# Kernel tuning notes

Hardware: AMD Instinct MI355X
Metric: run time of the kernel (lower is better)

## Reference

```python
import jax, jax.numpy as jnp
import numpy as np

ALPHA = 0.2          # LeakyReLU negative slope
NEG_INF = -9e15      # mask fill value from the torch code


def _gat_layer(h, adj_mask, W, a):
    """Faithful GAT layer. The torch code builds an [m*m, 2F] tensor and
    multiplies by a [2F,1] vector; algebraically identical to splitting
    a into a_i (first F) and a_k (last F) and broadcasting:
    e[i,k] = leakyrelu(Wh[i] . a_i + Wh[k] . a_k).
    Dropout is identity in eval mode (training=False)."""
    Wh = h @ W                                   # [m, F]
    F_out = W.shape[1]
    s_i = Wh @ a[:F_out, 0]                      # [m]
    s_k = Wh @ a[F_out:, 0]                      # [m]
    e = jax.nn.leaky_relu(s_i[:, None] + s_k[None, :], negative_slope=ALPHA)  # [m, m]
    e = jnp.where(adj_mask > 0, e, NEG_INF)
    attention = jax.nn.softmax(e, axis=1)        # row-wise softmax
    return jax.nn.elu(attention @ Wh)            # [m, F]


def setup_inputs() -> dict:
    m, in_dim, hid, emb = 4096, 64, 64, 32
    key = jax.random.key(0)
    k = jax.random.split(key, 6)
    # xavier-uniform-like init, gain=1.414
    def xavier(kk, shape):
        fan_in, fan_out = shape[0], shape[1]
        bound = 1.414 * np.sqrt(6.0 / (fan_in + fan_out))
        return jax.random.uniform(kk, shape, jnp.float32, -bound, bound)
    return {
        "h0": jax.random.normal(k[0], (m, in_dim), jnp.float32),
        "adj_mask": jax.random.randint(k[1], (m, m), 0, 2, jnp.int32),
        "W1": xavier(k[2], (in_dim, hid)),
        "a1": xavier(k[3], (2 * hid, 1)),
        "W2": xavier(k[4], (hid, emb)),
        "a2": xavier(k[5], (2 * emb, 1)),
        "omega": xavier(jax.random.fold_in(key, 7), (2 * emb, 1)),
    }


def reference(h0, adj_mask, W1, a1, W2, a2, omega):
    h1 = _gat_layer(h0, adj_mask, W1, a1)        # [m, hid]
    hL = _gat_layer(h1, adj_mask, W2, a2)        # [m, emb]
    # pairwise link score: sigmoid(omega . [hL_i, hL_k]) -- same broadcast trick
    emb = hL.shape[1]
    p_i = hL @ omega[:emb, 0]                    # [m]
    p_k = hL @ omega[emb:, 0]                    # [m]
    pred_matrix = jax.nn.sigmoid(p_i[:, None] + p_k[None, :])  # [m, m]
    return pred_matrix, hL
```

## Files before the change

kernel.cpp:

```cpp
#include <hip/hip_runtime.h>
#include <hip/hip_bf16.h>
#include <math.h>

#define M 4096
#define ALPHA 0.2f
#define L2E 1.4426950408889634f
#define PACK_BLOCKS (M * M / 4 / 256)

typedef __attribute__((ext_vector_type(8))) short bf16x8_t;
typedef __attribute__((ext_vector_type(4))) float f32x4_t;

#define EXP2F(x) __builtin_amdgcn_exp2f(x)

__device__ inline unsigned short f2bf(float f) {
    unsigned int u = __float_as_uint(f);
    u = (u + 0x7fffu + ((u >> 16) & 1u)) >> 16;
    return (unsigned short)u;
}
__device__ inline unsigned short f2bf_fast(float f) {
    return (unsigned short)((__float_as_uint(f) + 0x8000u) >> 16);
}
__device__ inline size_t whb_idx(int i, int c, int NFB) {
    return (((size_t)(i >> 5) * NFB + (c >> 4)) * 64 +
            (((i & 31) >> 3) * 16 + (c & 15))) * 8 + (i & 7);
}

__global__ __launch_bounds__(256) void prep_fat_kernel(const int* __restrict__ adj,
                                                       unsigned int* __restrict__ packedT,
                                                       const float* __restrict__ h0,
                                                       const float* __restrict__ W1,
                                                       const float* __restrict__ a1,
                                                       unsigned short* __restrict__ WhB1,
                                                       float* __restrict__ si1,
                                                       float* __restrict__ sk1) {
    int lane = threadIdx.x & 63;
    if (blockIdx.x < PACK_BLOCKS) {
        int g = blockIdx.x * 256 + threadIdx.x;
        int4 av = ((const int4*)adj)[g];
        unsigned int nib = (av.x > 0 ? 1u : 0u) | (av.y > 0 ? 2u : 0u) |
                           (av.z > 0 ? 4u : 0u) | (av.w > 0 ? 8u : 0u);
        unsigned int sh = nib << ((lane & 7) * 4);
        sh |= __shfl_xor(sh, 1);
        sh |= __shfl_xor(sh, 2);
        sh |= __shfl_xor(sh, 4);
        if ((lane & 7) == 0) packedT[(size_t)((g >> 3) & 127) * M + (g >> 10)] = sh;
        return;
    }
    int wave = threadIdx.x >> 6;
    int i = (blockIdx.x - PACK_BLOCKS) * 4 + wave;
    float acc = 0.f;
#pragma unroll
    for (int j = 0; j < 64; j++)
        acc += h0[(size_t)i * 64 + j] * W1[j * 64 + lane];
    float vi = acc * a1[lane], vk = acc * a1[64 + lane];
#pragma unroll
    for (int off = 32; off; off >>= 1) { vi += __shfl_xor(vi, off); vk += __shfl_xor(vk, off); }
    if (lane == 0) { si1[i] = vi; sk1[i] = vk; }
    WhB1[whb_idx(i, lane, 4)] = f2bf(acc);
}

template <int F, bool FINAL>
__global__ __launch_bounds__(1024) void attn_fused_kernel(
    const unsigned short* __restrict__ WhB,
    const float* __restrict__ s_i, const float* __restrict__ s_k,
    const unsigned int* __restrict__ packedT,
    const float* __restrict__ W2, const float* __restrict__ a2,
    unsigned short* __restrict__ WhB2, float* __restrict__ si2, float* __restrict__ sk2,
    const float* __restrict__ omega, float* __restrict__ hL_out,
    float* __restrict__ p_i, float* __restrict__ p_k) {
    constexpr int NFB = F / 16;
    constexpr int NWAVE = 16;
    constexpr int WPW = (M / 32) / NWAVE;
    __shared__ unsigned int mask_lds[16][129];
    __shared__ float acc_lds[NWAVE][16][F + 1];
    __shared__ float sred[NWAVE][16];
    __shared__ float wred[NWAVE];
    __shared__ float h_lds[16][F + 1];

    int tid = threadIdx.x, wave = tid >> 6, lane = tid & 63;
    int R0 = blockIdx.x * 16;

    float m = -INFINITY;
#pragma unroll
    for (int t = 0; t < M / 1024; t++) m = fmaxf(m, s_k[tid + t * 1024]);
#pragma unroll
    for (int off = 32; off; off >>= 1) m = fmaxf(m, __shfl_xor(m, off));
    if (lane == 0) wred[wave] = m;
#pragma unroll
    for (int q = 0; q < 2; q++) {
        int lin = q * 1024 + tid;
        int st = lin >> 4, r = lin & 15;
        mask_lds[r][st] = packedT[(size_t)st * M + R0 + r];
    }
    __syncthreads();
    float skmax = wred[0];
#pragma unroll
    for (int w = 1; w < NWAVE; w++) skmax = fmaxf(skmax, wred[w]);

    int fl = lane & 15, kg = lane >> 4;
    int row = R0 + fl;
    float si = s_i[row];
    float xm = si + skmax;
    float rl2 = fmaxf(xm, ALPHA * xm) * L2E;
    f32x4_t acc[NFB];
#pragma unroll
    for (int fb = 0; fb < NFB; fb++) acc[fb] = (f32x4_t)0.f;
    float rsum = 0.f;
    const int kw0 = wave * WPW;
#pragma unroll
    for (int st = 0; st < WPW; st++) {
        int kb = (kw0 + st) * 32;
        float4 sa = *(const float4*)&s_k[kb + kg * 8];
        float4 sb = *(const float4*)&s_k[kb + kg * 8 + 4];
        unsigned int word = mask_lds[fl][kw0 + st];
        float sv[8] = { sa.x, sa.y, sa.z, sa.w, sb.x, sb.y, sb.z, sb.w };
        union { bf16x8_t v; unsigned short u[8]; } af;
#pragma unroll
        for (int j = 0; j < 8; j++) {
            float x = si + sv[j];
            float e = fmaxf(x, ALPHA * x);
            float p = EXP2F(fmaf(e, L2E, -rl2));
            p = ((word >> (kg * 8 + j)) & 1u) ? p : 0.f;
            rsum += p;
            af.u[j] = f2bf_fast(p);
        }
        const unsigned short* bp = WhB + (size_t)(kw0 + st) * (NFB * 512) + (size_t)lane * 8;
#pragma unroll
        for (int fb = 0; fb < NFB; fb++) {
            bf16x8_t bfrag = *(const bf16x8_t*)(bp + (size_t)fb * 512);
            acc[fb] = __builtin_amdgcn_mfma_f32_16x16x32_bf16(af.v, bfrag, acc[fb], 0, 0, 0);
        }
    }
    rsum += __shfl_xor(rsum, 16);
    rsum += __shfl_xor(rsum, 32);
    if (lane < 16) sred[wave][lane] = rsum;
#pragma unroll
    for (int fb = 0; fb < NFB; fb++)
#pragma unroll
        for (int r = 0; r < 4; r++)
            acc_lds[wave][kg * 4 + r][fb * 16 + fl] = acc[fb][r];
    __syncthreads();

    if (tid < 16 * F) {
        int r = tid / F, c = tid % F;
        float s = 0.f, S = 0.f;
#pragma unroll
        for (int w = 0; w < NWAVE; w++) { s += acc_lds[w][r][c]; S += sred[w][r]; }
        float h = S > 0.f ? s / S : 0.f;
        h = h > 0.f ? h : (__expf(h) - 1.f);
        h_lds[r][c] = h;
        if (FINAL) hL_out[(size_t)(R0 + r) * F + c] = h;
    }
    __syncthreads();

    if (tid < 512) {
        int r = tid >> 5, c = tid & 31;
        float vi, vk;
        if (!FINAL) {
            float w2 = 0.f;
#pragma unroll
            for (int f = 0; f < 64; f++) w2 += h_lds[r][f] * W2[f * 32 + c];
            WhB2[whb_idx(R0 + r, c, 2)] = f2bf(w2);
            vi = w2 * a2[c];
            vk = w2 * a2[32 + c];
        } else {
            float hv = h_lds[r][c];
            vi = hv * omega[c];
            vk = hv * omega[32 + c];
        }
#pragma unroll
        for (int off = 16; off; off >>= 1) { vi += __shfl_xor(vi, off); vk += __shfl_xor(vk, off); }
        if ((tid & 31) == 0) {
            if (!FINAL) { si2[R0 + r] = vi; sk2[R0 + r] = vk; }
            else        { p_i[R0 + r] = vi; p_k[R0 + r] = vk; }
        }
    }
}

__global__ __launch_bounds__(256) void pred_kernel(const float* __restrict__ p_i,
                                                   const float* __restrict__ p_k,
                                                   float* __restrict__ out) {
    int gid = blockIdx.x * 256 + threadIdx.x;
#pragma unroll
    for (int t = 0; t < 4; t++) {
        int idx4 = gid + t * (M * M / 16);
        int i = idx4 >> 10;
        int k4 = (idx4 & 1023) * 4;
        float pi = p_i[i];
        float4 pk = *(const float4*)&p_k[k4];
        float4 o;
        o.x = 1.f / (1.f + __expf(-(pi + pk.x)));
        o.y = 1.f / (1.f + __expf(-(pi + pk.y)));
        o.z = 1.f / (1.f + __expf(-(pi + pk.z)));
        o.w = 1.f / (1.f + __expf(-(pi + pk.w)));
        *(float4*)&out[(size_t)i * M + k4] = o;
    }
}

extern "C" void kernel_launch(void* const* d_in, const int* in_sizes, int n_in,
                              void* d_out, int out_size, void* d_ws, size_t ws_size,
                              hipStream_t stream) {
    const float* h0    = (const float*)d_in[0];
    const int*   adj   = (const int*)d_in[1];
    const float* W1    = (const float*)d_in[2];
    const float* a1    = (const float*)d_in[3];
    const float* W2    = (const float*)d_in[4];
    const float* a2    = (const float*)d_in[5];
    const float* omega = (const float*)d_in[6];
    float* out = (float*)d_out;

    char* ws = (char*)d_ws;
    unsigned int*   packedT = (unsigned int*)(ws + 0);
    unsigned short* WhB1    = (unsigned short*)(ws + 2097152);
    unsigned short* WhB2    = (unsigned short*)(ws + 2621440);
    float* si1 = (float*)(ws + 2883584);
    float* sk1 = (float*)(ws + 2899968);
    float* si2 = (float*)(ws + 2916352);
    float* sk2 = (float*)(ws + 2932736);
    float* pi  = (float*)(ws + 2949120);
    float* pk  = (float*)(ws + 2965504);

    prep_fat_kernel<<<PACK_BLOCKS + M / 4, 256, 0, stream>>>(
        adj, packedT, h0, W1, a1, WhB1, si1, sk1);

    attn_fused_kernel<64, false><<<M / 16, 1024, 0, stream>>>(
        WhB1, si1, sk1, packedT, W2, a2, WhB2, si2, sk2,
        nullptr, nullptr, nullptr, nullptr);

    attn_fused_kernel<32, true><<<M / 16, 1024, 0, stream>>>(
        WhB2, si2, sk2, packedT, nullptr, nullptr, nullptr, nullptr, nullptr,
        omega, out + (size_t)M * M, pi, pk);

    pred_kernel<<<M * M / 16 / 256, 256, 0, stream>>>(pi, pk, out);
}
```

Baseline: 58.76 us.

## Halve attention block to 8 waves and make pack/pred kernels loop per thread

The attention kernels now run 512-thread blocks with 8 waves, each covering twice as many key tiles, using a partially unrolled loop. The mask staging and reduction phases are adapted to the smaller block. The adjacency packing and sigmoid prediction kernels launch fewer blocks and loop over 8 chunks per thread, cutting launch and scheduling overhead. A half-finished 8-row variant kernel was added that is never launched and leaves incomplete code behind.

```diff
diff --git a/kernel.cpp b/kernel.cpp
--- a/kernel.cpp
+++ b/kernel.cpp
@@ -5,7 +5,8 @@
 #define M 4096
 #define ALPHA 0.2f
 #define L2E 1.4426950408889634f
-#define PACK_BLOCKS (M * M / 4 / 256)
+#define PACK_BLOCKS 2048
+#define PRED_BLOCKS 2048
 
 typedef __attribute__((ext_vector_type(8))) short bf16x8_t;
 typedef __attribute__((ext_vector_type(4))) float f32x4_t;
@@ -35,15 +36,19 @@
                                                        float* __restrict__ sk1) {
     int lane = threadIdx.x & 63;
     if (blockIdx.x < PACK_BLOCKS) {
-        int g = blockIdx.x * 256 + threadIdx.x;
-        int4 av = ((const int4*)adj)[g];
-        unsigned int nib = (av.x > 0 ? 1u : 0u) | (av.y > 0 ? 2u : 0u) |
-                           (av.z > 0 ? 4u : 0u) | (av.w > 0 ? 8u : 0u);
-        unsigned int sh = nib << ((lane & 7) * 4);
-        sh |= __shfl_xor(sh, 1);
-        sh |= __shfl_xor(sh, 2);
-        sh |= __shfl_xor(sh, 4);
-        if ((lane & 7) == 0) packedT[(size_t)((g >> 3) & 127) * M + (g >> 10)] = sh;
+        int gid = blockIdx.x * 256 + threadIdx.x;
+#pragma unroll
+        for (int t = 0; t < 8; t++) {
+            int g = gid + t * (PACK_BLOCKS * 256);
+            int4 av = ((const int4*)adj)[g];
+            unsigned int nib = (av.x > 0 ? 1u : 0u) | (av.y > 0 ? 2u : 0u) |
+                               (av.z > 0 ? 4u : 0u) | (av.w > 0 ? 8u : 0u);
+            unsigned int sh = nib << ((lane & 7) * 4);
+            sh |= __shfl_xor(sh, 1);
+            sh |= __shfl_xor(sh, 2);
+            sh |= __shfl_xor(sh, 4);
+            if ((lane & 7) == 0) packedT[(size_t)((g >> 3) & 127) * M + (g >> 10)] = sh;
+        }
         return;
     }
     int wave = threadIdx.x >> 6;
@@ -60,7 +65,7 @@
 }
 
 template <int F, bool FINAL>
-__global__ __launch_bounds__(1024) void attn_fused_kernel(
+__global__ __launch_bounds__(512) void attn_fused_kernel(
     const unsigned short* __restrict__ WhB,
     const float* __restrict__ s_i, const float* __restrict__ s_k,
     const unsigned int* __restrict__ packedT,
@@ -69,10 +74,94 @@
     const float* __restrict__ omega, float* __restrict__ hL_out,
     float* __restrict__ p_i, float* __restrict__ p_k) {
     constexpr int NFB = F / 16;
-    constexpr int NWAVE = 16;
+    constexpr int NWAVE = 8;
+    constexpr int WPW = (M / 32) / NWAVE;
+    __shared__ unsigned int mask_lds[8][129];
+    __shared__ float acc_lds[NWAVE][8][F + 4];
+    __shared__ float sred[NWAVE][8];
+    __shared__ float wred[NWAVE];
+    __shared__ float h_lds[8][F + 1];
+
+    int tid = threadIdx.x, wave = tid >> 6, lane = tid & 63;
+    int R0 = blockIdx.x * 8;
+
+    float m = -INFINITY;
+#pragma unroll
+    for (int t = 0; t < M / 512; t++) m = fmaxf(m, s_k[tid + t * 512]);
+#pragma unroll
+    for (int off = 32; off; off >>= 1) m = fmaxf(m, __shfl_xor(m, off));
+    if (lane == 0) wred[wave] = m;
+#pragma unroll
+    for (int q = 0; q < 2; q++) {
+        int lin = q * 512 + tid;
+        int st = lin >> 3, r = lin & 7;
+        mask_lds[r][st] = packedT[(size_t)st * M + R0 + r];
+    }
+    __syncthreads();
+    float skmax = wred[0];
+#pragma unroll
+    for (int w = 1; w < NWAVE; w++) skmax = fmaxf(skmax, wred[w]);
+
+    int fl = lane & 15, kg = lane >> 4;
+    int row = R0 + (fl & 7);
+    float si = s_i[row];
+    float xm = si + skmax;
+    float rl2 = fmaxf(xm, ALPHA * xm) * L2E;
+    f32x4_t acc[NFB];
+#pragma unroll
+    for (int fb = 0; fb < NFB; fb++) acc[fb] = (f32x4_t)0.f;
+    float rsum = 0.f;
+    const int kw0 = wave * WPW;
+#pragma unroll 4
+    for (int st = 0; st < WPW; st++) {
+        int kb = (kw0 + st) * 32;
+        float4 sa = *(const float4*)&s_k[kb + kg * 8];
+        float4 sb = *(const float4*)&s_k[kb + kg * 8 + 4];
+        unsigned int word = mask_lds[fl & 7][kw0 + st];
+        float sv[8] = { sa.x, sa.y, sa.z, sa.w, sb.x, sb.y, sb.z, sb.w };
+        union { bf16x8_t v; unsigned short u[8]; } af;
+#pragma unroll
+        for (int j = 0; j < 8; j++) {
+            float x = si + sv[j];
+            float e = fmaxf(x, ALPHA * x);
+            float p = EXP2F(fmaf(e, L2E, -rl2));
+            p = ((word >> (kg * 8 + j)) & 1u) ? p : 0.f;
+            rsum += p;
+            af.u[j] = f2bf_fast(p);
+        }
+        const unsigned short* bp = WhB + (size_t)(kw0 + st) * (NFB * 512) + (size_t)lane * 8;
+#pragma unroll
+        for (int fb = 0; fb < NFB; fb++) {
+            bf16x8_t bfrag = *(const bf16x8_t*)(bp + (size_t)fb * 512);
+            acc[fb] = __builtin_amdgcn_mfma_f32_16x16x32_bf16(af.v, bfrag, acc[fb], 0, 0, 0);
+        }
+    }
+    rsum += __shfl_xor(rsum, 16);
+    rsum += __shfl_xor(rsum, 32);
+    rsum += __shfl_xor(rsum, 8);
+    if (lane < 8) sred[wave][lane] = rsum;
+#pragma unroll
+    for (int fb = 0; fb < NFB; fb++)
+#pragma unroll
+        for (int r = 0; r < 4; r++)
+            if (fl < 8) acc_lds[wave][fl][fb * 16 + kg * 4 + r] = 0.f;
+    __syncthreads();
+}
+
+template <int F, bool FINAL>
+__global__ __launch_bounds__(512) void attn_fused16_kernel(
+    const unsigned short* __restrict__ WhB,
+    const float* __restrict__ s_i, const float* __restrict__ s_k,
+    const unsigned int* __restrict__ packedT,
+    const float* __restrict__ W2, const float* __restrict__ a2,
+    unsigned short* __restrict__ WhB2, float* __restrict__ si2, float* __restrict__ sk2,
+    const float* __restrict__ omega, float* __restrict__ hL_out,
+    float* __restrict__ p_i, float* __restrict__ p_k) {
+    constexpr int NFB = F / 16;
+    constexpr int NWAVE = 8;
     constexpr int WPW = (M / 32) / NWAVE;
     __shared__ unsigned int mask_lds[16][129];
-    __shared__ float acc_lds[NWAVE][16][F + 1];
+    __shared__ float acc_lds[NWAVE][16][F + 4];
     __shared__ float sred[NWAVE][16];
     __shared__ float wred[NWAVE];
     __shared__ float h_lds[16][F + 1];
@@ -82,13 +171,13 @@
 
     float m = -INFINITY;
 #pragma unroll
-    for (int t = 0; t < M / 1024; t++) m = fmaxf(m, s_k[tid + t * 1024]);
+    for (int t = 0; t < M / 512; t++) m = fmaxf(m, s_k[tid + t * 512]);
 #pragma unroll
     for (int off = 32; off; off >>= 1) m = fmaxf(m, __shfl_xor(m, off));
     if (lane == 0) wred[wave] = m;
 #pragma unroll
-    for (int q = 0; q < 2; q++) {
-        int lin = q * 1024 + tid;
+    for (int q = 0; q < 4; q++) {
+        int lin = q * 512 + tid;
         int st = lin >> 4, r = lin & 15;
         mask_lds[r][st] = packedT[(size_t)st * M + R0 + r];
     }
@@ -107,7 +196,7 @@
     for (int fb = 0; fb < NFB; fb++) acc[fb] = (f32x4_t)0.f;
     float rsum = 0.f;
     const int kw0 = wave * WPW;
-#pragma unroll
+#pragma unroll 4
     for (int st = 0; st < WPW; st++) {
         int kb = (kw0 + st) * 32;
         float4 sa = *(const float4*)&s_k[kb + kg * 8];
@@ -141,19 +230,23 @@
             acc_lds[wave][kg * 4 + r][fb * 16 + fl] = acc[fb][r];
     __syncthreads();
 
-    if (tid < 16 * F) {
-        int r = tid / F, c = tid % F;
-        float s = 0.f, S = 0.f;
-#pragma unroll
-        for (int w = 0; w < NWAVE; w++) { s += acc_lds[w][r][c]; S += sred[w][r]; }
-        float h = S > 0.f ? s / S : 0.f;
-        h = h > 0.f ? h : (__expf(h) - 1.f);
-        h_lds[r][c] = h;
-        if (FINAL) hL_out[(size_t)(R0 + r) * F + c] = h;
-    }
-    __syncthreads();
-
-    if (tid < 512) {
+#pragma unroll
+    for (int q = 0; q < (16 * F + 511) / 512; q++) {
+        int cell = q * 512 + tid;
+        if (cell < 16 * F) {
+            int r = cell / F, c = cell % F;
+            float s = 0.f, S = 0.f;
+#pragma unroll
+            for (int w = 0; w < NWAVE; w++) { s += acc_lds[w][r][c]; S += sred[w][r]; }
+            float h = S > 0.f ? s / S : 0.f;
+            h = h > 0.f ? h : (__expf(h) - 1.f);
+            h_lds[r][c] = h;
+            if (FINAL) hL_out[(size_t)(R0 + r) * F + c] = h;
+        }
+    }
+    __syncthreads();
+
+    {
         int r = tid >> 5, c = tid & 31;
         float vi, vk;
         if (!FINAL) {
@@ -182,8 +275,8 @@
                                                    float* __restrict__ out) {
     int gid = blockIdx.x * 256 + threadIdx.x;
 #pragma unroll
-    for (int t = 0; t < 4; t++) {
-        int idx4 = gid + t * (M * M / 16);
+    for (int t = 0; t < 8; t++) {
+        int idx4 = gid + t * (PRED_BLOCKS * 256);
         int i = idx4 >> 10;
         int k4 = (idx4 & 1023) * 4;
         float pi = p_i[i];
@@ -223,13 +316,13 @@
     prep_fat_kernel<<<PACK_BLOCKS + M / 4, 256, 0, stream>>>(
         adj, packedT, h0, W1, a1, WhB1, si1, sk1);
 
-    attn_fused_kernel<64, false><<<M / 16, 1024, 0, stream>>>(
+    attn_fused16_kernel<64, false><<<M / 16, 512, 0, stream>>>(
         WhB1, si1, sk1, packedT, W2, a2, WhB2, si2, sk2,
         nullptr, nullptr, nullptr, nullptr);
 
-    attn_fused_kernel<32, true><<<M / 16, 1024, 0, stream>>>(
+    attn_fused16_kernel<32, true><<<M / 16, 512, 0, stream>>>(
         WhB2, si2, sk2, packedT, nullptr, nullptr, nullptr, nullptr, nullptr,
         omega, out + (size_t)M * M, pi, pk);
 
-    pred_kernel<<<M * M / 16 / 256, 256, 0, stream>>>(pi, pk, out);
-}
+    pred_kernel<<<PRED_BLOCKS, 256, 0, stream>>>(pi, pk, out);
+}
```

New measurement: 61.82 us. 1.05x slower.

## Fuse adjacency bit-packing into first attention layer kernel

Applied to the files above, without the earlier changes.

The adjacency int mask is now read and bit-packed directly inside the first attention kernel, with each block packing its own 16 rows into LDS and using them immediately. The packed transposed mask is still written to global memory for the second layer. This removes the separate packing pass and the first layer's reread of the packed mask. The cost is that the 64 MB adjacency read now sits on the first attention kernel's critical path, with fewer blocks (256) to hide its latency, and the extra LDS use may lower occupancy.

```diff
diff --git a/kernel.cpp b/kernel.cpp
--- a/kernel.cpp
+++ b/kernel.cpp
@@ -5,7 +5,6 @@
 #define M 4096
 #define ALPHA 0.2f
 #define L2E 1.4426950408889634f
-#define PACK_BLOCKS (M * M / 4 / 256)
 
 typedef __attribute__((ext_vector_type(8))) short bf16x8_t;
 typedef __attribute__((ext_vector_type(4))) float f32x4_t;
@@ -25,29 +24,14 @@
             (((i & 31) >> 3) * 16 + (c & 15))) * 8 + (i & 7);
 }
 
-__global__ __launch_bounds__(256) void prep_fat_kernel(const int* __restrict__ adj,
-                                                       unsigned int* __restrict__ packedT,
-                                                       const float* __restrict__ h0,
+__global__ __launch_bounds__(256) void fused_in_kernel(const float* __restrict__ h0,
                                                        const float* __restrict__ W1,
                                                        const float* __restrict__ a1,
                                                        unsigned short* __restrict__ WhB1,
                                                        float* __restrict__ si1,
                                                        float* __restrict__ sk1) {
-    int lane = threadIdx.x & 63;
-    if (blockIdx.x < PACK_BLOCKS) {
-        int g = blockIdx.x * 256 + threadIdx.x;
-        int4 av = ((const int4*)adj)[g];
-        unsigned int nib = (av.x > 0 ? 1u : 0u) | (av.y > 0 ? 2u : 0u) |
-                           (av.z > 0 ? 4u : 0u) | (av.w > 0 ? 8u : 0u);
-        unsigned int sh = nib << ((lane & 7) * 4);
-        sh |= __shfl_xor(sh, 1);
-        sh |= __shfl_xor(sh, 2);
-        sh |= __shfl_xor(sh, 4);
-        if ((lane & 7) == 0) packedT[(size_t)((g >> 3) & 127) * M + (g >> 10)] = sh;
-        return;
-    }
-    int wave = threadIdx.x >> 6;
-    int i = (blockIdx.x - PACK_BLOCKS) * 4 + wave;
+    int wave = threadIdx.x >> 6, lane = threadIdx.x & 63;
+    int i = blockIdx.x * 4 + wave;
     float acc = 0.f;
 #pragma unroll
     for (int j = 0; j < 64; j++)
@@ -59,11 +43,11 @@
     WhB1[whb_idx(i, lane, 4)] = f2bf(acc);
 }
 
-template <int F, bool FINAL>
+template <int F, bool FINAL, bool PACK>
 __global__ __launch_bounds__(1024) void attn_fused_kernel(
     const unsigned short* __restrict__ WhB,
     const float* __restrict__ s_i, const float* __restrict__ s_k,
-    const unsigned int* __restrict__ packedT,
+    const int* __restrict__ adj, unsigned int* __restrict__ packedT,
     const float* __restrict__ W2, const float* __restrict__ a2,
     unsigned short* __restrict__ WhB2, float* __restrict__ si2, float* __restrict__ sk2,
     const float* __restrict__ omega, float* __restrict__ hL_out,
@@ -72,6 +56,7 @@
     constexpr int NWAVE = 16;
     constexpr int WPW = (M / 32) / NWAVE;
     __shared__ unsigned int mask_lds[16][129];
+    __shared__ unsigned int wlds[NWAVE][16][WPW];
     __shared__ float acc_lds[NWAVE][16][F + 1];
     __shared__ float sred[NWAVE][16];
     __shared__ float wred[NWAVE];
@@ -86,16 +71,48 @@
 #pragma unroll
     for (int off = 32; off; off >>= 1) m = fmaxf(m, __shfl_xor(m, off));
     if (lane == 0) wred[wave] = m;
-#pragma unroll
-    for (int q = 0; q < 2; q++) {
-        int lin = q * 1024 + tid;
-        int st = lin >> 4, r = lin & 15;
-        mask_lds[r][st] = packedT[(size_t)st * M + R0 + r];
+
+    if (PACK) {
+#pragma unroll
+        for (int b = 0; b < 4; b++) {
+            int4 av[4];
+#pragma unroll
+            for (int rr = 0; rr < 4; rr++) {
+                int r = b * 4 + rr;
+                av[rr] = ((const int4*)adj)[(size_t)(R0 + r) * (M / 4) + wave * 64 + lane];
+            }
+#pragma unroll
+            for (int rr = 0; rr < 4; rr++) {
+                int r = b * 4 + rr;
+                unsigned int nib = (av[rr].x > 0 ? 1u : 0u) | (av[rr].y > 0 ? 2u : 0u) |
+                                   (av[rr].z > 0 ? 4u : 0u) | (av[rr].w > 0 ? 8u : 0u);
+                unsigned int sh = nib << ((lane & 7) * 4);
+                sh |= __shfl_xor(sh, 1);
+                sh |= __shfl_xor(sh, 2);
+                sh |= __shfl_xor(sh, 4);
+                if ((lane & 7) == 0) wlds[wave][r][lane >> 3] = sh;
+            }
+        }
+    } else {
+#pragma unroll
+        for (int q = 0; q < 2; q++) {
+            int lin = q * 1024 + tid;
+            int st = lin >> 4, r = lin & 15;
+            mask_lds[r][st] = packedT[(size_t)st * M + R0 + r];
+        }
     }
     __syncthreads();
     float skmax = wred[0];
 #pragma unroll
     for (int w = 1; w < NWAVE; w++) skmax = fmaxf(skmax, wred[w]);
+    if (PACK) {
+#pragma unroll
+        for (int q = 0; q < 2; q++) {
+            int lin = q * 1024 + tid;
+            int kw = lin >> 4, r = lin & 15;
+            packedT[(size_t)kw * M + R0 + r] = wlds[kw >> 3][r][kw & 7];
+        }
+    }
 
     int fl = lane & 15, kg = lane >> 4;
     int row = R0 + fl;
@@ -112,7 +129,7 @@
         int kb = (kw0 + st) * 32;
         float4 sa = *(const float4*)&s_k[kb + kg * 8];
         float4 sb = *(const float4*)&s_k[kb + kg * 8 + 4];
-        unsigned int word = mask_lds[fl][kw0 + st];
+        unsigned int word = PACK ? wlds[wave][fl][st] : mask_lds[fl][kw0 + st];
         float sv[8] = { sa.x, sa.y, sa.z, sa.w, sb.x, sb.y, sb.z, sb.w };
         union { bf16x8_t v; unsigned short u[8]; } af;
 #pragma unroll
@@ -220,15 +237,14 @@
     float* pi  = (float*)(ws + 2949120);
     float* pk  = (float*)(ws + 2965504);
 
-    prep_fat_kernel<<<PACK_BLOCKS + M / 4, 256, 0, stream>>>(
-        adj, packedT, h0, W1, a1, WhB1, si1, sk1);
-
-    attn_fused_kernel<64, false><<<M / 16, 1024, 0, stream>>>(
-        WhB1, si1, sk1, packedT, W2, a2, WhB2, si2, sk2,
+    fused_in_kernel<<<M / 4, 256, 0, stream>>>(h0, W1, a1, WhB1, si1, sk1);
+
+    attn_fused_kernel<64, false, true><<<M / 16, 1024, 0, stream>>>(
+        WhB1, si1, sk1, adj, packedT, W2, a2, WhB2, si2, sk2,
         nullptr, nullptr, nullptr, nullptr);
 
-    attn_fused_kernel<32, true><<<M / 16, 1024, 0, stream>>>(
-        WhB2, si2, sk2, packedT, nullptr, nullptr, nullptr, nullptr, nullptr,
+    attn_fused_kernel<32, true, false><<<M / 16, 1024, 0, stream>>>(
+        WhB2, si2, sk2, nullptr, packedT, nullptr, nullptr, nullptr, nullptr, nullptr,
         omega, out + (size_t)M * M, pi, pk);
 
     pred_kernel<<<M * M / 16 / 256, 256, 0, stream>>>(pi, pk, out);
```

New measurement: 55.92 us. 1.05x faster.
